# Performance work log

Measured on AMD Instinct MI355X. Metric: run time of the kernel, lower is better.

## Reference

```python
import jax, jax.numpy as jnp
import numpy as np

N_WAY, K_SHOT = 5, 1
N_CLASSES = 64
D = 8


def _conv(x, w, b):
    y = jax.lax.conv_general_dilated(x, w, (2, 2), 'SAME',
                                     dimension_numbers=('NCHW', 'OIHW', 'NCHW'))
    return jax.nn.relu(y + b[None, :, None, None])


def setup_inputs() -> dict:
    key = jax.random.key(0)
    ks = jax.random.split(key, 12)
    b, s_sup, q, h, w = 4, N_WAY * K_SHOT, 1, 64, 64
    rnd = lambda k, shape: jax.random.normal(k, shape, jnp.float32) * 0.05
    return {
        'support_x': jax.random.normal(ks[0], (b, s_sup, 3, h, w), jnp.float32),
        'support_y': jax.random.randint(ks[1], (b, s_sup), 0, N_CLASSES),
        'query_x': jax.random.normal(ks[2], (b, q, 3, h, w), jnp.float32),
        'query_y': jax.random.randint(ks[3], (b, q), 0, N_CLASSES),
        'k1': rnd(ks[4], (32, 3, 3, 3)), 'bc1': jnp.zeros((32,), jnp.float32),
        'k2': rnd(ks[5], (48, 32, 3, 3)), 'bc2': jnp.zeros((48,), jnp.float32),
        'k3': rnd(ks[6], (64, 48, 3, 3)), 'bc3': jnp.zeros((64,), jnp.float32),
        'Wlog': rnd(ks[7], (64, N_CLASSES)), 'blog': jnp.zeros((N_CLASSES,), jnp.float32),
        'Wg1': rnd(ks[8], (132, 128)), 'bg1': jnp.zeros((128,), jnp.float32),
        'Wg2': rnd(ks[9], (128, 64)), 'bg2': jnp.zeros((64,), jnp.float32),
        'Wf1': rnd(ks[10], (64, 16)), 'bf1': jnp.zeros((16,), jnp.float32),
        'Wf2': rnd(ks[11], (16, 1)), 'bf2': jnp.zeros((1,), jnp.float32),
    }


def reference(support_x, support_y, query_x, query_y,
              k1, bc1, k2, bc2, k3, bc3, Wlog, blog,
              Wg1, bg1, Wg2, bg2, Wf1, bf1, Wf2, bf2):
    x = jnp.concatenate([support_x, query_x], axis=1)       # [b, s, 3, h, w]
    label = jnp.concatenate([support_y, query_y], axis=1)   # [b, s]
    b, s = label.shape
    h, w = x.shape[-2:]

    feat = x.reshape(b * s, 3, h, w)
    feat = _conv(feat, k1, bc1)
    feat = _conv(feat, k2, bc2)
    feat = _conv(feat, k3, bc3)                              # [b*s, c, D, D]
    c = feat.shape[1]
    logits = feat.mean(axis=(2, 3)) @ Wlog + blog            # [b*s, n_classes]

    # --- append normalized (i/d, j/d) coord channels ---
    ii = jnp.arange(D, dtype=feat.dtype) / D
    coord = jnp.stack([jnp.broadcast_to(ii[:, None], (D, D)),
                       jnp.broadcast_to(ii[None, :], (D, D))])        # [2, D, D]
    feat = feat.reshape(b, s, c, D, D)
    feat = jnp.concatenate([feat, jnp.broadcast_to(coord, (b, s, 2, D, D))], axis=2)
    c2 = c + 2
    m = D * D
    a = feat.reshape(b, s, c2, m).transpose(0, 1, 3, 2)      # [b, s, m, c2]

    # --- relation network g over all (set-pair, position-pair) combos ---
    # original: g(concat(x_i, x_j)) where x_i = x[b, j, :, q], x_j = x[b, i, :, p]
    # split first linear: concat @ Wg1 = x_i @ Wg1[:c2] + x_j @ Wg1[c2:]
    W1a, W1b = Wg1[:c2], Wg1[c2:]
    u = a @ W1a                                              # [b, s_j, m_q, 128]
    v = a @ W1b + bg1                                        # [b, s_i, m_p, 128]
    # hdd[b,i,j,q,p] = relu(u[b,j,q] + v[b,i,p])  -> [b, s, s, m, m, 128]
    hdd = jax.nn.relu(u[:, None, :, :, None, :] + v[:, :, None, None, :, :])
    g = jax.nn.relu(hdd @ Wg2 + bg2)                         # [b, s, s, m, m, 64]
    x_f = g.sum(axis=(3, 4))                                 # [b, s, s, 64]
    score = jax.nn.sigmoid(jax.nn.relu(x_f @ Wf1 + bf1) @ Wf2 + bf2)  # [b, s, s, 1]

    # --- losses ---
    logp = jax.nn.log_softmax(logits, axis=-1)
    lab = label.reshape(-1)
    cls_loss = -jnp.take_along_axis(logp, lab[:, None], axis=1).mean()

    y = (label[:, :, None] == label[:, None, :])[..., None].astype(score.dtype)
    P = score[..., 0]                                        # [b, s, s]
    Pt = P.transpose(0, 2, 1)
    sym, anti = 0.5 * (P + Pt), 0.5 * (P - Pt)
    sym_n = jnp.sqrt((sym ** 2).sum(axis=(1, 2)))            # Frobenius per batch
    anti_n = jnp.sqrt((anti ** 2).sum(axis=(1, 2)))
    sym_loss = ((sym_n - anti_n) / (sym_n + anti_n)).mean()
    euc_loss = ((score - y) ** 2).mean()
    rn_loss = euc_loss - 0.1 * sym_loss
    return (cls_loss, rn_loss, sym_loss)
```

## Files before the change

### kernel.cpp

```cpp
#include <hip/hip_runtime.h>

typedef _Float16 f16x8 __attribute__((ext_vector_type(8)));
typedef float f32x4 __attribute__((ext_vector_type(4)));

__device__ unsigned g_rel_done = 0;
__device__ unsigned g_c3[24] = {};


__global__ void __launch_bounds__(256) conv1_k(
        const float* __restrict__ sx, const float* __restrict__ qx,
        const float* __restrict__ w, const float* __restrict__ bias,
        float* __restrict__ out,
        const float* __restrict__ Wg2, _Float16* __restrict__ W2h) {
    if (blockIdx.x == 96) {
        for (int s = 0; s < 4; s++) {
            int slot = threadIdx.x + 256*s;
            int tile = slot >> 6, lane = slot & 63;
            int kt = tile >> 2, nt = tile & 3;
            int quad = lane >> 4, col = lane & 15;
            f16x8 t;
            #pragma unroll
            for (int jj = 0; jj < 8; jj++)
                t[jj] = (_Float16)Wg2[(kt*32 + quad*8 + jj)*64 + nt*16 + col];
            *(f16x8*)&W2h[slot*8] = t;
        }
        return;
    }
    int r8 = blockIdx.x & 7, q = blockIdx.x >> 3;
    int n    = (q >> 2)*8 + r8;
    int oc0  = (q & 3)*8;
    int bi = n / 6, si = n % 6;
    const float* inp = (si < 5) ? sx + (size_t)((bi*5+si)*3)*4096
                                : qx + (size_t)(bi*3)*4096;
    __shared__ __align__(16) float ish[3*4352];
    __shared__ float wl[216];
    __shared__ float bl[8];
    const int tid = threadIdx.x;
    #pragma unroll
    for (int j = 0; j < 12; j++) {
        int k = tid + j*256;
        f32x4 t = *(const f32x4*)&inp[k*4];
        int plane = k >> 10, rem = k & 1023, row = rem >> 4, c4 = (rem & 15)*4;
        *(f32x4*)&ish[plane*4352 + row*68 + c4] = t;
    }
    if (tid < 216) wl[tid] = w[oc0*27 + tid];
    if (tid >= 240 && tid < 248) bl[tid-240] = bias[oc0 + tid - 240];
    __syncthreads();
    for (int s = 0; s < 4; s++) {
        int idx = tid + s*256;
        int oy = idx >> 5, ox = idx & 31;
        float tap[27];
        #pragma unroll
        for (int ic = 0; ic < 3; ic++)
            #pragma unroll
            for (int dy = 0; dy < 3; dy++) {
                int iy = 2*oy + dy;
                #pragma unroll
                for (int dx = 0; dx < 3; dx++) {
                    int ix = 2*ox + dx;
                    tap[ic*9+dy*3+dx] = (iy < 64 && ix < 64)
                                      ? ish[ic*4352 + iy*68 + ix] : 0.f;
                }
            }
        #pragma unroll
        for (int o = 0; o < 8; o++) {
            float acc = bl[o];
            #pragma unroll
            for (int t = 0; t < 27; t++) acc += tap[t]*wl[o*27 + t];
            out[(size_t)(n*32 + oc0 + o)*1024 + idx] = fmaxf(acc, 0.f);
        }
    }
}

__global__ void __launch_bounds__(256) conv2_k(
        const float* __restrict__ in, const float* __restrict__ w,
        const float* __restrict__ bias, float* __restrict__ out) {
    int r8 = blockIdx.x & 7, q = blockIdx.x >> 3;
    int n   = (q / 12)*8 + r8;
    int ocg = q % 12;
    __shared__ __align__(16) float wl[1152];
    __shared__ __align__(16) float pin[16*1152];
    const int tid = threadIdx.x;
    const float* ib = in + (size_t)n*32*1024;
    #pragma unroll
    for (int j = 0; j < 16; j++) {
        int k = tid + j*256;
        f32x4 t = *(const f32x4*)&ib[k*4];
        int s = k >> 8, rem = k & 255, row = rem >> 3, c4 = (rem & 7)*4;
        *(f32x4*)&pin[s*1152 + row*36 + c4] = t;
    }
    f32x4 rb[16];
    #pragma unroll
    for (int j = 0; j < 16; j++) {
        int k = tid + j*256;
        rb[j] = *(const f32x4*)&ib[16384 + k*4];
    }
    for (int e = tid; e < 288; e += 256)
        *(f32x4*)&wl[e*4] = *(const f32x4*)&w[ocg*1152 + e*4];
    __syncthreads();
    int oy = tid >> 4, ox = tid & 15;
    float a0 = bias[ocg*4+0], a1 = bias[ocg*4+1];
    float a2 = bias[ocg*4+2], a3 = bias[ocg*4+3];
    #pragma unroll 4
    for (int ic = 0; ic < 16; ic++) {
        const float* pp = &pin[ic*1152];
        float tap[9];
        #pragma unroll
        for (int dy = 0; dy < 3; dy++)
            #pragma unroll
            for (int dx = 0; dx < 3; dx++) {
                int iy = 2*oy+dy, ix = 2*ox+dx;
                tap[dy*3+dx] = (iy < 32 && ix < 32) ? pp[iy*36 + ix] : 0.f;
            }
        #pragma unroll
        for (int t = 0; t < 9; t++) {
            a0 += tap[t]*wl[0*288 + ic*9 + t];
            a1 += tap[t]*wl[1*288 + ic*9 + t];
            a2 += tap[t]*wl[2*288 + ic*9 + t];
            a3 += tap[t]*wl[3*288 + ic*9 + t];
        }
    }
    __syncthreads();
    #pragma unroll
    for (int j = 0; j < 16; j++) {
        int k = tid + j*256;
        int s = k >> 8, rem = k & 255, row = rem >> 3, c4 = (rem & 7)*4;
        *(f32x4*)&pin[s*1152 + row*36 + c4] = rb[j];
    }
    __syncthreads();
    #pragma unroll 4
    for (int ic = 16; ic < 32; ic++) {
        const float* pp = &pin[(ic-16)*1152];
        float tap[9];
        #pragma unroll
        for (int dy = 0; dy < 3; dy++)
            #pragma unroll
            for (int dx = 0; dx < 3; dx++) {
                int iy = 2*oy+dy, ix = 2*ox+dx;
                tap[dy*3+dx] = (iy < 32 && ix < 32) ? pp[iy*36 + ix] : 0.f;
            }
        #pragma unroll
        for (int t = 0; t < 9; t++) {
            a0 += tap[t]*wl[0*288 + ic*9 + t];
            a1 += tap[t]*wl[1*288 + ic*9 + t];
            a2 += tap[t]*wl[2*288 + ic*9 + t];
            a3 += tap[t]*wl[3*288 + ic*9 + t];
        }
    }
    size_t ob = (size_t)(n*48 + ocg*4)*256 + tid;
    out[ob        ] = fmaxf(a0, 0.f);
    out[ob + 256  ] = fmaxf(a1, 0.f);
    out[ob + 512  ] = fmaxf(a2, 0.f);
    out[ob + 768  ] = fmaxf(a3, 0.f);
}

__global__ void __launch_bounds__(256) conv3uv_k(
        const float* __restrict__ feat2, const float* __restrict__ k3w,
        const float* __restrict__ bc3, float* __restrict__ feat3g,
        float* __restrict__ mf,
        const float* __restrict__ Wg1, const float* __restrict__ bg1,
        _Float16* __restrict__ u16, _Float16* __restrict__ v16,
        const int* __restrict__ sy, const int* __restrict__ qy,
        const float* __restrict__ Wlog, const float* __restrict__ blog,
        float* __restrict__ rv) {
    __shared__ __align__(16) float smem[18816];
    __shared__ unsigned Rsh;
    const int tid = threadIdx.x;
    int r8 = blockIdx.x & 7, q = blockIdx.x >> 3;
    int n = (q >> 3)*8 + r8;
    int L = q & 7;

    float* pin3 = smem;
    float* wl3  = smem + 15360;
    {
        const float* ib = feat2 + (size_t)n*48*256;
        #pragma unroll
        for (int j = 0; j < 12; j++) {
            int k = tid + j*256;
            f32x4 t = *(const f32x4*)&ib[k*4];
            int plane = k >> 6, rem = k & 63, row = rem >> 2, c4 = (rem & 3)*4;
            *(f32x4*)&pin3[plane*320 + row*20 + c4] = t;
        }
    }
    for (int e = tid; e < 864; e += 256)
        *(f32x4*)&wl3[e*4] = *(const f32x4*)&k3w[L*3456 + e*4];
    __syncthreads();
    int pix = tid & 63, osub = tid >> 6;
    int oy = pix >> 3, ox = pix & 7;
    int ol0 = osub*2;
    float a0 = bc3[L*8 + ol0], a1 = bc3[L*8 + ol0 + 1];
    #pragma unroll 4
    for (int ic = 0; ic < 48; ic++) {
        const float* pp = &pin3[ic*320];
        float tap[9];
        #pragma unroll
        for (int dy = 0; dy < 3; dy++)
            #pragma unroll
            for (int dx = 0; dx < 3; dx++) {
                int iy = 2*oy+dy, ix = 2*ox+dx;
                tap[dy*3+dx] = (iy < 16 && ix < 16) ? pp[iy*20 + ix] : 0.f;
            }
        #pragma unroll
        for (int t = 0; t < 9; t++) {
            a0 += tap[t]*wl3[ ol0   *432 + ic*9 + t];
            a1 += tap[t]*wl3[(ol0+1)*432 + ic*9 + t];
        }
    }
    float r0 = fmaxf(a0, 0.f), r1 = fmaxf(a1, 0.f);
    __hip_atomic_store(&feat3g[(size_t)(n*64 + L*8 + ol0  )*64 + pix], r0,
                       __ATOMIC_RELAXED, __HIP_MEMORY_SCOPE_AGENT);
    __hip_atomic_store(&feat3g[(size_t)(n*64 + L*8 + ol0+1)*64 + pix], r1,
                       __ATOMIC_RELAXED, __HIP_MEMORY_SCOPE_AGENT);
    #pragma unroll
    for (int off = 32; off >= 1; off >>= 1) {
        r0 += __shfl_xor(r0, off, 64);
        r1 += __shfl_xor(r1, off, 64);
    }
    if (pix == 0) {
        __hip_atomic_store(&mf[n*64 + L*8 + ol0    ], r0 * (1.f/64.f),
                           __ATOMIC_RELAXED, __HIP_MEMORY_SCOPE_AGENT);
        __hip_atomic_store(&mf[n*64 + L*8 + ol0 + 1], r1 * (1.f/64.f),
                           __ATOMIC_RELAXED, __HIP_MEMORY_SCOPE_AGENT);
    }
    asm volatile("s_waitcnt vmcnt(0)" ::: "memory");
    __syncthreads();
    if (tid == 0) {
        unsigned my = __hip_atomic_fetch_add(&g_c3[n], 1u, __ATOMIC_RELAXED,
                                             __HIP_MEMORY_SCOPE_AGENT) + 1u;
        Rsh = (my + 7u) / 8u;
    }
    __syncthreads();
    const unsigned R = Rsh;
    if (tid == 0) {
        while (__hip_atomic_load(&g_c3[n], __ATOMIC_RELAXED,
                                 __HIP_MEMORY_SCOPE_AGENT) < R*8u)
            __builtin_amdgcn_s_sleep(2);
    }
    __syncthreads();

    {
        int half = tid >> 7, t = tid & 127;
        int pg = L*2 + half;
        float* a4 = smem + half*264;
        for (int e = t; e < 264; e += 128) {
            int pl = e / 66, c = e % 66;
            int p = pg*4 + pl;
            float vv;
            if (c < 64)
                vv = __hip_atomic_load(&feat3g[(size_t)(n*64 + c)*64 + p],
                                       __ATOMIC_RELAXED, __HIP_MEMORY_SCOPE_AGENT);
            else if (c == 64) vv = (float)(p >> 3) * 0.125f;
            else              vv = (float)(p & 7) * 0.125f;
            a4[pl*66 + c] = vv;
        }
        __syncthreads();
        float us[4] = {0.f,0.f,0.f,0.f};
        float bg = bg1[t];
        float vs[4] = {bg,bg,bg,bg};
        for (int c = 0; c < 66; c++) {
            float wa = Wg1[c*128 + t];
            float wb = Wg1[(66+c)*128 + t];
            #pragma unroll
            for (int pl = 0; pl < 4; pl++) {
                us[pl] += a4[pl*66 + c]*wa;
                vs[pl] += a4[pl*66 + c]*wb;
            }
        }
        #pragma unroll
        for (int pl = 0; pl < 4; pl++) {
            int p = pg*4 + pl;
            u16[(size_t)(n*64+p)*128 + t] = (_Float16)us[pl];
            v16[(size_t)(n*64+p)*128 + t] = (_Float16)vs[pl];
        }
    }

    if (L == 0 && tid < 64) {
        float s = blog[tid];
        for (int c = 0; c < 64; c++)
            s += __hip_atomic_load(&mf[n*64 + c], __ATOMIC_RELAXED,
                                   __HIP_MEMORY_SCOPE_AGENT) * Wlog[c*64 + tid];
        float mx = s;
        #pragma unroll
        for (int off = 32; off >= 1; off >>= 1) mx = fmaxf(mx, __shfl_xor(mx, off, 64));
        float p = __expf(s - mx);
        float se = p;
        #pragma unroll
        for (int off = 32; off >= 1; off >>= 1) se += __shfl_xor(se, off, 64);
        int bi = n/6, si = n%6;
        int lab = (si < 5) ? sy[bi*5+si] : qy[bi];
        float s_lab = __shfl(s, lab, 64);
        if (tid == 0) rv[n] = -(s_lab - mx - __logf(se));
    }
}

__global__ void __launch_bounds__(256, 2) rel_k(
        const _Float16* __restrict__ U, const _Float16* __restrict__ V,
        const _Float16* __restrict__ W2h, const float* __restrict__ bg2,
        float* __restrict__ xfpT,
        const float* __restrict__ rv,
        const int* __restrict__ sy, const int* __restrict__ qy,
        const float* __restrict__ Wf1, const float* __restrict__ bf1,
        const float* __restrict__ Wf2, const float* __restrict__ bf2,
        float* __restrict__ out) {
    __shared__ __align__(16) float smem[1792];
    __shared__ unsigned lastflag;
    _Float16* Vsh   = (_Float16*)smem;
    float*    xfred = smem + 1024;

    int r8 = blockIdx.x & 7, qq = blockIdx.x >> 3;
    int b = r8 >> 1;
    int m = (qq << 1) | (r8 & 1);
    int cb = m >> 2, qc = m & 3;
    int j = cb / 6, i = cb % 6;
    int tid  = threadIdx.x;
    int wv   = tid >> 6, lane = tid & 63;
    int col  = lane & 15, quad = lane >> 4;

    const _Float16* ub = U + (size_t)(b*6 + i)*8192;
    const _Float16* vb = V + (size_t)(b*6 + j)*8192 + qc*16*128;

    *(f16x8*)&Vsh[tid*8] = *(const f16x8*)&vb[tid*8];

    f16x8 uf[4];
    {
        const _Float16* up = ub + (wv*16 + col)*128 + quad*8;
        #pragma unroll
        for (int kt = 0; kt < 4; kt++) uf[kt] = *(const f16x8*)&up[kt*32];
    }
    f16x8 bf[4][4];
    #pragma unroll
    for (int kt = 0; kt < 4; kt++)
        #pragma unroll
        for (int nt = 0; nt < 4; nt++)
            bf[kt][nt] = *(const f16x8*)&W2h[(size_t)(((kt*4+nt)*64) + lane)*8];
    float bgv[4];
    #pragma unroll
    for (int nt = 0; nt < 4; nt++) bgv[nt] = bg2[nt*16 + col];

    __syncthreads();

    float sums[4] = {0.f,0.f,0.f,0.f};
    for (int qi = 0; qi < 16; qi++) {
        const _Float16* vp = &Vsh[qi*128 + quad*8];
        f32x4 acc[4];
        #pragma unroll
        for (int nt = 0; nt < 4; nt++)
            acc[nt] = (f32x4){bgv[nt], bgv[nt], bgv[nt], bgv[nt]};
        #pragma unroll
        for (int kt = 0; kt < 4; kt++) {
            f16x8 vf = *(const f16x8*)&vp[kt*32];
            f16x8 af = uf[kt] + vf;
            af = __builtin_elementwise_max(af, (f16x8){0,0,0,0,0,0,0,0});
            #pragma unroll
            for (int nt = 0; nt < 4; nt++)
                acc[nt] = __builtin_amdgcn_mfma_f32_16x16x32_f16(af, bf[kt][nt], acc[nt], 0, 0, 0);
        }
        #pragma unroll
        for (int nt = 0; nt < 4; nt++)
            #pragma unroll
            for (int rr = 0; rr < 4; rr++)
                sums[nt] += fmaxf(acc[nt][rr], 0.f);
    }

    #pragma unroll
    for (int nt = 0; nt < 4; nt++) {
        sums[nt] += __shfl_xor(sums[nt], 16, 64);
        sums[nt] += __shfl_xor(sums[nt], 32, 64);
    }
    if (lane < 16) {
        #pragma unroll
        for (int nt = 0; nt < 4; nt++) xfred[wv*64 + nt*16 + lane] = sums[nt];
    }
    __syncthreads();
    if (tid < 64) {
        float val = xfred[tid] + xfred[64+tid] + xfred[128+tid] + xfred[192+tid];
        __hip_atomic_store(&xfpT[(size_t)tid*576 + (unsigned)(b*144 + m)], val,
                           __ATOMIC_RELAXED, __HIP_MEMORY_SCOPE_AGENT);
    }
    if (wv == 0) asm volatile("s_waitcnt vmcnt(0)" ::: "memory");
    if (tid == 0) {
        unsigned my = __hip_atomic_fetch_add(&g_rel_done, 1u, __ATOMIC_RELAXED,
                                             __HIP_MEMORY_SCOPE_AGENT);
        lastflag = ((my % 576u) == 575u) ? 1u : 0u;
    }
    __syncthreads();
    if (!lastflag) return;

    {
        float* Wf1sh = smem;
        float* wf2sh = smem + 1024;
        float* bf1sh = smem + 1040;
        float* Pm    = smem + 1056;
        int*   lab   = (int*)(smem + 1200);
        float* red   = smem + 1232;
        float* ratio = smem + 1488;
        for (int e = tid; e < 1024; e += 256) Wf1sh[e] = Wf1[e];
        if (tid < 16) { wf2sh[tid] = Wf2[tid]; bf1sh[tid] = bf1[tid]; }
        if (tid < 24) { int bi = tid/6, si = tid%6; lab[tid] = (si < 5) ? sy[bi*5+si] : qy[bi]; }
        __syncthreads();
        if (tid < 144) {
            float hid[16];
            #pragma unroll
            for (int h = 0; h < 16; h++) hid[h] = bf1sh[h];
            for (int nn = 0; nn < 64; nn++) {
                const float* xp = &xfpT[(size_t)nn*576 + tid*4];
                float x = 0.f;
                #pragma unroll
                for (int c = 0; c < 4; c++)
                    x += __hip_atomic_load(&xp[c], __ATOMIC_RELAXED,
                                           __HIP_MEMORY_SCOPE_AGENT);
                #pragma unroll
                for (int h = 0; h < 16; h++) hid[h] += x * Wf1sh[nn*16 + h];
            }
            float sc = bf2[0];
            #pragma unroll
            for (int h = 0; h < 16; h++) sc += fmaxf(hid[h], 0.f) * wf2sh[h];
            Pm[tid] = 1.f/(1.f + __expf(-sc));
        }
        __syncthreads();
        float e = 0.f;
        if (tid < 144) {
            int bb = tid/36, r = tid%36, jj = r/6, ii = r%6;
            float y = (lab[bb*6+jj] == lab[bb*6+ii]) ? 1.f : 0.f;
            float d = Pm[tid] - y;
            e = d*d;
        }
        red[tid] = e;
        __syncthreads();
        for (int s = 128; s > 0; s >>= 1) {
            if (tid < s) red[tid] += red[tid+s];
            __syncthreads();
        }
        if (tid < 4) {
            float s2 = 0.f, a2 = 0.f;
            for (int jj = 0; jj < 6; jj++)
                for (int ii = 0; ii < 6; ii++) {
                    float pa = Pm[tid*36 + jj*6 + ii], pb = Pm[tid*36 + ii*6 + jj];
                    float sm = 0.5f*(pa+pb), an = 0.5f*(pa-pb);
                    s2 += sm*sm; a2 += an*an;
                }
            float sn = sqrtf(s2), anq = sqrtf(a2);
            ratio[tid] = (sn - anq)/(sn + anq);
        }
        __syncthreads();
        if (tid == 0) {
            float sl = 0.25f*(ratio[0]+ratio[1]+ratio[2]+ratio[3]);
            float euc = red[0] * (1.f/144.f);
            float cs = 0.f;
            for (int k = 0; k < 24; k++) cs += rv[k];
            out[0] = cs * (1.f/24.f);
            out[1] = euc - 0.1f*sl;
            out[2] = sl;
        }
    }
}

extern "C" void kernel_launch(void* const* d_in, const int* in_sizes, int n_in,
                              void* d_out, int out_size, void* d_ws, size_t ws_size,
                              hipStream_t stream) {
    const float* sx   = (const float*)d_in[0];
    const int*   sy   = (const int*)  d_in[1];
    const float* qx   = (const float*)d_in[2];
    const int*   qy   = (const int*)  d_in[3];
    const float* k1   = (const float*)d_in[4];
    const float* bc1  = (const float*)d_in[5];
    const float* k2   = (const float*)d_in[6];
    const float* bc2  = (const float*)d_in[7];
    const float* k3   = (const float*)d_in[8];
    const float* bc3  = (const float*)d_in[9];
    const float* Wlog = (const float*)d_in[10];
    const float* blog = (const float*)d_in[11];
    const float* Wg1  = (const float*)d_in[12];
    const float* bg1  = (const float*)d_in[13];
    const float* Wg2  = (const float*)d_in[14];
    const float* bg2  = (const float*)d_in[15];
    const float* Wf1  = (const float*)d_in[16];
    const float* bf1  = (const float*)d_in[17];
    const float* Wf2  = (const float*)d_in[18];
    const float* bf2  = (const float*)d_in[19];

    float* ws    = (float*)d_ws;
    float* feat1 = ws;
    float* feat2 = feat1 + 786432;
    float* feat3 = feat2 + 294912;
    float* mf    = feat3 + 98304;
    float* rv    = mf    + 1536;
    float* xfpT  = rv    + 32;
    _Float16* u16 = (_Float16*)(xfpT + 36864);
    _Float16* v16 = u16 + 196608;
    _Float16* W2h = v16 + 196608;
    float* out   = (float*)d_out;

    conv1_k   <<<97,  256, 0, stream>>>(sx, qx, k1, bc1, feat1, Wg2, W2h);
    conv2_k   <<<288, 256, 0, stream>>>(feat1, k2, bc2, feat2);
    conv3uv_k <<<192, 256, 0, stream>>>(feat2, k3, bc3, feat3, mf,
                                        Wg1, bg1, u16, v16, sy, qy, Wlog, blog, rv);
    rel_k     <<<576, 256, 0, stream>>>(u16, v16, W2h, bg2, xfpT,
                                        rv, sy, qy, Wf1, bf1, Wf2, bf2, out);
}
```

Measured before the change: 168.9 us.

## Fuse conv2 into conv3uv kernel with per-sample spin barrier; shrink rel grid

Merges the conv2 kernel into the conv3/uv kernel. Each of the 8 blocks per sample computes 6 conv2 output channels, publishes them with atomic stores, and waits on a per-sample counter before loading the full feat2 for conv3. This removes one kernel launch and its inter-kernel gap. The relation kernel drops from 576 to 144 blocks, with each block looping over 4 query chunks and reloading the V tile into shared memory. The fused kernel now relies on co-residency spin-waits, and the relation stage has less parallelism per launch.

```diff
diff --git a/kernel.cpp b/kernel.cpp
--- a/kernel.cpp
+++ b/kernel.cpp
@@ -4,6 +4,7 @@
 typedef float f32x4 __attribute__((ext_vector_type(4)));
 
 __device__ unsigned g_rel_done = 0;
+__device__ unsigned g_c2[24] = {};
 __device__ unsigned g_c3[24] = {};
 
 
@@ -72,166 +73,169 @@
     }
 }
 
-__global__ void __launch_bounds__(256) conv2_k(
-        const float* __restrict__ in, const float* __restrict__ w,
-        const float* __restrict__ bias, float* __restrict__ out) {
-    int r8 = blockIdx.x & 7, q = blockIdx.x >> 3;
-    int n   = (q / 12)*8 + r8;
-    int ocg = q % 12;
-    __shared__ __align__(16) float wl[1152];
-    __shared__ __align__(16) float pin[16*1152];
-    const int tid = threadIdx.x;
-    const float* ib = in + (size_t)n*32*1024;
-    #pragma unroll
-    for (int j = 0; j < 16; j++) {
-        int k = tid + j*256;
-        f32x4 t = *(const f32x4*)&ib[k*4];
-        int s = k >> 8, rem = k & 255, row = rem >> 3, c4 = (rem & 7)*4;
-        *(f32x4*)&pin[s*1152 + row*36 + c4] = t;
-    }
-    f32x4 rb[16];
-    #pragma unroll
-    for (int j = 0; j < 16; j++) {
-        int k = tid + j*256;
-        rb[j] = *(const f32x4*)&ib[16384 + k*4];
-    }
-    for (int e = tid; e < 288; e += 256)
-        *(f32x4*)&wl[e*4] = *(const f32x4*)&w[ocg*1152 + e*4];
-    __syncthreads();
-    int oy = tid >> 4, ox = tid & 15;
-    float a0 = bias[ocg*4+0], a1 = bias[ocg*4+1];
-    float a2 = bias[ocg*4+2], a3 = bias[ocg*4+3];
-    #pragma unroll 4
-    for (int ic = 0; ic < 16; ic++) {
-        const float* pp = &pin[ic*1152];
-        float tap[9];
-        #pragma unroll
-        for (int dy = 0; dy < 3; dy++)
-            #pragma unroll
-            for (int dx = 0; dx < 3; dx++) {
-                int iy = 2*oy+dy, ix = 2*ox+dx;
-                tap[dy*3+dx] = (iy < 32 && ix < 32) ? pp[iy*36 + ix] : 0.f;
-            }
-        #pragma unroll
-        for (int t = 0; t < 9; t++) {
-            a0 += tap[t]*wl[0*288 + ic*9 + t];
-            a1 += tap[t]*wl[1*288 + ic*9 + t];
-            a2 += tap[t]*wl[2*288 + ic*9 + t];
-            a3 += tap[t]*wl[3*288 + ic*9 + t];
-        }
-    }
-    __syncthreads();
-    #pragma unroll
-    for (int j = 0; j < 16; j++) {
-        int k = tid + j*256;
-        int s = k >> 8, rem = k & 255, row = rem >> 3, c4 = (rem & 7)*4;
-        *(f32x4*)&pin[s*1152 + row*36 + c4] = rb[j];
-    }
-    __syncthreads();
-    #pragma unroll 4
-    for (int ic = 16; ic < 32; ic++) {
-        const float* pp = &pin[(ic-16)*1152];
-        float tap[9];
-        #pragma unroll
-        for (int dy = 0; dy < 3; dy++)
-            #pragma unroll
-            for (int dx = 0; dx < 3; dx++) {
-                int iy = 2*oy+dy, ix = 2*ox+dx;
-                tap[dy*3+dx] = (iy < 32 && ix < 32) ? pp[iy*36 + ix] : 0.f;
-            }
-        #pragma unroll
-        for (int t = 0; t < 9; t++) {
-            a0 += tap[t]*wl[0*288 + ic*9 + t];
-            a1 += tap[t]*wl[1*288 + ic*9 + t];
-            a2 += tap[t]*wl[2*288 + ic*9 + t];
-            a3 += tap[t]*wl[3*288 + ic*9 + t];
-        }
-    }
-    size_t ob = (size_t)(n*48 + ocg*4)*256 + tid;
-    out[ob        ] = fmaxf(a0, 0.f);
-    out[ob + 256  ] = fmaxf(a1, 0.f);
-    out[ob + 512  ] = fmaxf(a2, 0.f);
-    out[ob + 768  ] = fmaxf(a3, 0.f);
-}
-
-__global__ void __launch_bounds__(256) conv3uv_k(
-        const float* __restrict__ feat2, const float* __restrict__ k3w,
-        const float* __restrict__ bc3, float* __restrict__ feat3g,
-        float* __restrict__ mf,
+__global__ void __launch_bounds__(256) c23uv_k(
+        const float* __restrict__ feat1, const float* __restrict__ k2w,
+        const float* __restrict__ bc2, float* __restrict__ feat2,
+        const float* __restrict__ k3w, const float* __restrict__ bc3,
+        float* __restrict__ feat3g, float* __restrict__ mf,
         const float* __restrict__ Wg1, const float* __restrict__ bg1,
         _Float16* __restrict__ u16, _Float16* __restrict__ v16,
         const int* __restrict__ sy, const int* __restrict__ qy,
         const float* __restrict__ Wlog, const float* __restrict__ blog,
         float* __restrict__ rv) {
-    __shared__ __align__(16) float smem[18816];
+    __shared__ __align__(16) float smem[20160];
     __shared__ unsigned Rsh;
     const int tid = threadIdx.x;
     int r8 = blockIdx.x & 7, q = blockIdx.x >> 3;
     int n = (q >> 3)*8 + r8;
     int L = q & 7;
 
-    float* pin3 = smem;
-    float* wl3  = smem + 15360;
     {
-        const float* ib = feat2 + (size_t)n*48*256;
-        #pragma unroll
-        for (int j = 0; j < 12; j++) {
+        float* wl  = smem;
+        float* pin = smem + 1728;
+        const float* ib = feat1 + (size_t)n*32*1024;
+        #pragma unroll
+        for (int j = 0; j < 16; j++) {
             int k = tid + j*256;
             f32x4 t = *(const f32x4*)&ib[k*4];
-            int plane = k >> 6, rem = k & 63, row = rem >> 2, c4 = (rem & 3)*4;
-            *(f32x4*)&pin3[plane*320 + row*20 + c4] = t;
-        }
-    }
-    for (int e = tid; e < 864; e += 256)
-        *(f32x4*)&wl3[e*4] = *(const f32x4*)&k3w[L*3456 + e*4];
-    __syncthreads();
-    int pix = tid & 63, osub = tid >> 6;
-    int oy = pix >> 3, ox = pix & 7;
-    int ol0 = osub*2;
-    float a0 = bc3[L*8 + ol0], a1 = bc3[L*8 + ol0 + 1];
-    #pragma unroll 4
-    for (int ic = 0; ic < 48; ic++) {
-        const float* pp = &pin3[ic*320];
-        float tap[9];
-        #pragma unroll
-        for (int dy = 0; dy < 3; dy++)
-            #pragma unroll
-            for (int dx = 0; dx < 3; dx++) {
-                int iy = 2*oy+dy, ix = 2*ox+dx;
-                tap[dy*3+dx] = (iy < 16 && ix < 16) ? pp[iy*20 + ix] : 0.f;
-            }
-        #pragma unroll
-        for (int t = 0; t < 9; t++) {
-            a0 += tap[t]*wl3[ ol0   *432 + ic*9 + t];
-            a1 += tap[t]*wl3[(ol0+1)*432 + ic*9 + t];
-        }
-    }
-    float r0 = fmaxf(a0, 0.f), r1 = fmaxf(a1, 0.f);
-    __hip_atomic_store(&feat3g[(size_t)(n*64 + L*8 + ol0  )*64 + pix], r0,
-                       __ATOMIC_RELAXED, __HIP_MEMORY_SCOPE_AGENT);
-    __hip_atomic_store(&feat3g[(size_t)(n*64 + L*8 + ol0+1)*64 + pix], r1,
-                       __ATOMIC_RELAXED, __HIP_MEMORY_SCOPE_AGENT);
-    #pragma unroll
-    for (int off = 32; off >= 1; off >>= 1) {
-        r0 += __shfl_xor(r0, off, 64);
-        r1 += __shfl_xor(r1, off, 64);
-    }
-    if (pix == 0) {
-        __hip_atomic_store(&mf[n*64 + L*8 + ol0    ], r0 * (1.f/64.f),
-                           __ATOMIC_RELAXED, __HIP_MEMORY_SCOPE_AGENT);
-        __hip_atomic_store(&mf[n*64 + L*8 + ol0 + 1], r1 * (1.f/64.f),
-                           __ATOMIC_RELAXED, __HIP_MEMORY_SCOPE_AGENT);
+            int s = k >> 8, rem = k & 255, row = rem >> 3, c4 = (rem & 7)*4;
+            *(f32x4*)&pin[s*1152 + row*36 + c4] = t;
+        }
+        f32x4 rb[16];
+        #pragma unroll
+        for (int j = 0; j < 16; j++) {
+            int k = tid + j*256;
+            rb[j] = *(const f32x4*)&ib[16384 + k*4];
+        }
+        for (int e = tid; e < 432; e += 256)
+            *(f32x4*)&wl[e*4] = *(const f32x4*)&k2w[L*1728 + e*4];
+        __syncthreads();
+        int oy = tid >> 4, ox = tid & 15;
+        float a[6];
+        #pragma unroll
+        for (int o = 0; o < 6; o++) a[o] = bc2[L*6 + o];
+        #pragma unroll 4
+        for (int ic = 0; ic < 16; ic++) {
+            const float* pp = &pin[ic*1152];
+            float tap[9];
+            #pragma unroll
+            for (int dy = 0; dy < 3; dy++)
+                #pragma unroll
+                for (int dx = 0; dx < 3; dx++) {
+                    int iy = 2*oy+dy, ix = 2*ox+dx;
+                    tap[dy*3+dx] = (iy < 32 && ix < 32) ? pp[iy*36 + ix] : 0.f;
+                }
+            #pragma unroll
+            for (int t = 0; t < 9; t++)
+                #pragma unroll
+                for (int o = 0; o < 6; o++)
+                    a[o] += tap[t]*wl[o*288 + ic*9 + t];
+        }
+        __syncthreads();
+        #pragma unroll
+        for (int j = 0; j < 16; j++) {
+            int k = tid + j*256;
+            int s = k >> 8, rem = k & 255, row = rem >> 3, c4 = (rem & 7)*4;
+            *(f32x4*)&pin[s*1152 + row*36 + c4] = rb[j];
+        }
+        __syncthreads();
+        #pragma unroll 4
+        for (int ic = 16; ic < 32; ic++) {
+            const float* pp = &pin[(ic-16)*1152];
+            float tap[9];
+            #pragma unroll
+            for (int dy = 0; dy < 3; dy++)
+                #pragma unroll
+                for (int dx = 0; dx < 3; dx++) {
+                    int iy = 2*oy+dy, ix = 2*ox+dx;
+                    tap[dy*3+dx] = (iy < 32 && ix < 32) ? pp[iy*36 + ix] : 0.f;
+                }
+            #pragma unroll
+            for (int t = 0; t < 9; t++)
+                #pragma unroll
+                for (int o = 0; o < 6; o++)
+                    a[o] += tap[t]*wl[o*288 + ic*9 + t];
+        }
+        size_t ob = (size_t)(n*48 + L*6)*256 + tid;
+        #pragma unroll
+        for (int o = 0; o < 6; o++)
+            __hip_atomic_store(&feat2[ob + (size_t)o*256], fmaxf(a[o], 0.f),
+                               __ATOMIC_RELAXED, __HIP_MEMORY_SCOPE_AGENT);
     }
     asm volatile("s_waitcnt vmcnt(0)" ::: "memory");
     __syncthreads();
     if (tid == 0) {
-        unsigned my = __hip_atomic_fetch_add(&g_c3[n], 1u, __ATOMIC_RELAXED,
+        unsigned my = __hip_atomic_fetch_add(&g_c2[n], 1u, __ATOMIC_RELAXED,
                                              __HIP_MEMORY_SCOPE_AGENT) + 1u;
         Rsh = (my + 7u) / 8u;
     }
     __syncthreads();
     const unsigned R = Rsh;
     if (tid == 0) {
+        while (__hip_atomic_load(&g_c2[n], __ATOMIC_RELAXED,
+                                 __HIP_MEMORY_SCOPE_AGENT) < R*8u)
+            __builtin_amdgcn_s_sleep(2);
+    }
+    __syncthreads();
+
+    {
+        float* pin3 = smem;
+        float* wl3  = smem + 15360;
+        const float* f2 = feat2 + (size_t)n*48*256;
+        #pragma unroll 8
+        for (int jj = 0; jj < 48; jj++) {
+            int k = tid + jj*256;
+            float vIn = __hip_atomic_load(&f2[k], __ATOMIC_RELAXED,
+                                          __HIP_MEMORY_SCOPE_AGENT);
+            int plane = k >> 8, rem = k & 255, row = rem >> 4, cc = rem & 15;
+            pin3[plane*320 + row*20 + cc] = vIn;
+        }
+        for (int e = tid; e < 864; e += 256)
+            *(f32x4*)&wl3[e*4] = *(const f32x4*)&k3w[L*3456 + e*4];
+        __syncthreads();
+        int pix = tid & 63, osub = tid >> 6;
+        int oy = pix >> 3, ox = pix & 7;
+        int ol0 = osub*2;
+        float a0 = bc3[L*8 + ol0], a1 = bc3[L*8 + ol0 + 1];
+        #pragma unroll 4
+        for (int ic = 0; ic < 48; ic++) {
+            const float* pp = &pin3[ic*320];
+            float tap[9];
+            #pragma unroll
+            for (int dy = 0; dy < 3; dy++)
+                #pragma unroll
+                for (int dx = 0; dx < 3; dx++) {
+                    int iy = 2*oy+dy, ix = 2*ox+dx;
+                    tap[dy*3+dx] = (iy < 16 && ix < 16) ? pp[iy*20 + ix] : 0.f;
+                }
+            #pragma unroll
+            for (int t = 0; t < 9; t++) {
+                a0 += tap[t]*wl3[ ol0   *432 + ic*9 + t];
+                a1 += tap[t]*wl3[(ol0+1)*432 + ic*9 + t];
+            }
+        }
+        float r0 = fmaxf(a0, 0.f), r1 = fmaxf(a1, 0.f);
+        __hip_atomic_store(&feat3g[(size_t)(n*64 + L*8 + ol0  )*64 + pix], r0,
+                           __ATOMIC_RELAXED, __HIP_MEMORY_SCOPE_AGENT);
+        __hip_atomic_store(&feat3g[(size_t)(n*64 + L*8 + ol0+1)*64 + pix], r1,
+                           __ATOMIC_RELAXED, __HIP_MEMORY_SCOPE_AGENT);
+        #pragma unroll
+        for (int off = 32; off >= 1; off >>= 1) {
+            r0 += __shfl_xor(r0, off, 64);
+            r1 += __shfl_xor(r1, off, 64);
+        }
+        if (pix == 0) {
+            __hip_atomic_store(&mf[n*64 + L*8 + ol0    ], r0 * (1.f/64.f),
+                               __ATOMIC_RELAXED, __HIP_MEMORY_SCOPE_AGENT);
+            __hip_atomic_store(&mf[n*64 + L*8 + ol0 + 1], r1 * (1.f/64.f),
+                               __ATOMIC_RELAXED, __HIP_MEMORY_SCOPE_AGENT);
+        }
+    }
+    asm volatile("s_waitcnt vmcnt(0)" ::: "memory");
+    __syncthreads();
+    if (tid == 0) {
+        __hip_atomic_fetch_add(&g_c3[n], 1u, __ATOMIC_RELAXED,
+                               __HIP_MEMORY_SCOPE_AGENT);
         while (__hip_atomic_load(&g_c3[n], __ATOMIC_RELAXED,
                                  __HIP_MEMORY_SCOPE_AGENT) < R*8u)
             __builtin_amdgcn_s_sleep(2);
@@ -309,17 +313,14 @@
 
     int r8 = blockIdx.x & 7, qq = blockIdx.x >> 3;
     int b = r8 >> 1;
-    int m = (qq << 1) | (r8 & 1);
-    int cb = m >> 2, qc = m & 3;
-    int j = cb / 6, i = cb % 6;
+    int m2 = (qq << 1) | (r8 & 1);
+    int j = m2 / 6, i = m2 % 6;
     int tid  = threadIdx.x;
     int wv   = tid >> 6, lane = tid & 63;
     int col  = lane & 15, quad = lane >> 4;
 
     const _Float16* ub = U + (size_t)(b*6 + i)*8192;
-    const _Float16* vb = V + (size_t)(b*6 + j)*8192 + qc*16*128;
-
-    *(f16x8*)&Vsh[tid*8] = *(const f16x8*)&vb[tid*8];
+    const _Float16* vb0 = V + (size_t)(b*6 + j)*8192;
 
     f16x8 uf[4];
     {
@@ -337,51 +338,53 @@
     #pragma unroll
     for (int nt = 0; nt < 4; nt++) bgv[nt] = bg2[nt*16 + col];
 
-    __syncthreads();
-
-    float sums[4] = {0.f,0.f,0.f,0.f};
-    for (int qi = 0; qi < 16; qi++) {
-        const _Float16* vp = &Vsh[qi*128 + quad*8];
-        f32x4 acc[4];
-        #pragma unroll
-        for (int nt = 0; nt < 4; nt++)
-            acc[nt] = (f32x4){bgv[nt], bgv[nt], bgv[nt], bgv[nt]};
-        #pragma unroll
-        for (int kt = 0; kt < 4; kt++) {
-            f16x8 vf = *(const f16x8*)&vp[kt*32];
-            f16x8 af = uf[kt] + vf;
-            af = __builtin_elementwise_max(af, (f16x8){0,0,0,0,0,0,0,0});
+    for (int qc = 0; qc < 4; qc++) {
+        __syncthreads();
+        *(f16x8*)&Vsh[tid*8] = *(const f16x8*)&vb0[qc*2048 + tid*8];
+        __syncthreads();
+        float sums[4] = {0.f,0.f,0.f,0.f};
+        for (int qi = 0; qi < 16; qi++) {
+            const _Float16* vp = &Vsh[qi*128 + quad*8];
+            f32x4 acc[4];
             #pragma unroll
             for (int nt = 0; nt < 4; nt++)
-                acc[nt] = __builtin_amdgcn_mfma_f32_16x16x32_f16(af, bf[kt][nt], acc[nt], 0, 0, 0);
-        }
-        #pragma unroll
-        for (int nt = 0; nt < 4; nt++)
-            #pragma unroll
-            for (int rr = 0; rr < 4; rr++)
-                sums[nt] += fmaxf(acc[nt][rr], 0.f);
-    }
-
-    #pragma unroll
-    for (int nt = 0; nt < 4; nt++) {
-        sums[nt] += __shfl_xor(sums[nt], 16, 64);
-        sums[nt] += __shfl_xor(sums[nt], 32, 64);
-    }
-    if (lane < 16) {
-        #pragma unroll
-        for (int nt = 0; nt < 4; nt++) xfred[wv*64 + nt*16 + lane] = sums[nt];
-    }
-    __syncthreads();
-    if (tid < 64) {
-        float val = xfred[tid] + xfred[64+tid] + xfred[128+tid] + xfred[192+tid];
-        __hip_atomic_store(&xfpT[(size_t)tid*576 + (unsigned)(b*144 + m)], val,
-                           __ATOMIC_RELAXED, __HIP_MEMORY_SCOPE_AGENT);
+                acc[nt] = (f32x4){bgv[nt], bgv[nt], bgv[nt], bgv[nt]};
+            #pragma unroll
+            for (int kt = 0; kt < 4; kt++) {
+                f16x8 vf = *(const f16x8*)&vp[kt*32];
+                f16x8 af = uf[kt] + vf;
+                af = __builtin_elementwise_max(af, (f16x8){0,0,0,0,0,0,0,0});
+                #pragma unroll
+                for (int nt = 0; nt < 4; nt++)
+                    acc[nt] = __builtin_amdgcn_mfma_f32_16x16x32_f16(af, bf[kt][nt], acc[nt], 0, 0, 0);
+            }
+            #pragma unroll
+            for (int nt = 0; nt < 4; nt++)
+                #pragma unroll
+                for (int rr = 0; rr < 4; rr++)
+                    sums[nt] += fmaxf(acc[nt][rr], 0.f);
+        }
+        #pragma unroll
+        for (int nt = 0; nt < 4; nt++) {
+            sums[nt] += __shfl_xor(sums[nt], 16, 64);
+            sums[nt] += __shfl_xor(sums[nt], 32, 64);
+        }
+        if (lane < 16) {
+            #pragma unroll
+            for (int nt = 0; nt < 4; nt++) xfred[wv*64 + nt*16 + lane] = sums[nt];
+        }
+        __syncthreads();
+        if (tid < 64) {
+            float val = xfred[tid] + xfred[64+tid] + xfred[128+tid] + xfred[192+tid];
+            __hip_atomic_store(&xfpT[(size_t)tid*576 + (unsigned)(b*144 + m2*4 + qc)],
+                               val, __ATOMIC_RELAXED, __HIP_MEMORY_SCOPE_AGENT);
+        }
     }
     if (wv == 0) asm volatile("s_waitcnt vmcnt(0)" ::: "memory");
     if (tid == 0) {
         unsigned my = __hip_atomic_fetch_add(&g_rel_done, 1u, __ATOMIC_RELAXED,
                                              __HIP_MEMORY_SCOPE_AGENT);
-        lastflag = ((my % 576u) == 575u) ? 1u : 0u;
+        lastflag = ((my % 144u) == 143u) ? 1u : 0u;
     }
     __syncthreads();
     if (!lastflag) return;
@@ -491,10 +494,9 @@
     _Float16* W2h = v16 + 196608;
     float* out   = (float*)d_out;
 
-    conv1_k   <<<97,  256, 0, stream>>>(sx, qx, k1, bc1, feat1, Wg2, W2h);
-    conv2_k   <<<288, 256, 0, stream>>>(feat1, k2, bc2, feat2);
-    conv3uv_k <<<192, 256, 0, stream>>>(feat2, k3, bc3, feat3, mf,
-                                        Wg1, bg1, u16, v16, sy, qy, Wlog, blog, rv);
-    rel_k     <<<576, 256, 0, stream>>>(u16, v16, W2h, bg2, xfpT,
-                                        rv, sy, qy, Wf1, bf1, Wf2, bf2, out);
+    conv1_k <<<97,  256, 0, stream>>>(sx, qx, k1, bc1, feat1, Wg2, W2h);
+    c23uv_k <<<192, 256, 0, stream>>>(feat1, k2, bc2, feat2, k3, bc3, feat3, mf,
+                                      Wg1, bg1, u16, v16, sy, qy, Wlog, blog, rv);
+    rel_k   <<<144, 256, 0, stream>>>(u16, v16, W2h, bg2, xfpT,
+                                      rv, sy, qy, Wf1, bf1, Wf2, bf2, out);
 }
```

After: 183.9 us. +8.9%, slower.
